# Kernel tuning notes

Measured on AMD Instinct MI355X. Metric: run time of the kernel, lower is better.

## Reference

```python
import jax, jax.numpy as jnp
import numpy as np

N_NODES = 50000
N_EDGES = 800000
N_GRAPHS = 128
IN_CH = 16
IN_CTX = 16
H_G = 128
H_C = 128
H_F = 128


def _lin_init(key, fan_in, fan_out):
    k1, k2 = jax.random.split(key)
    s = 1.0 / np.sqrt(fan_in)
    W = jax.random.uniform(k1, (fan_in, fan_out), minval=-s, maxval=s, dtype=jnp.float32)
    b = jax.random.uniform(k2, (fan_out,), minval=-s, maxval=s, dtype=jnp.float32)
    return W, b


def setup_inputs() -> dict:
    key = jax.random.key(0)
    ks = jax.random.split(key, 16)
    inp = {}
    inp['x'] = jax.random.normal(ks[0], (N_NODES, IN_CH), dtype=jnp.float32)
    inp['x_context'] = jax.random.normal(ks[1], (N_GRAPHS, IN_CTX), dtype=jnp.float32)
    inp['edge_index'] = jax.random.randint(ks[2], (2, N_EDGES), 0, N_NODES, dtype=jnp.int64)
    inp['batch'] = jnp.sort(jax.random.randint(ks[3], (N_NODES,), 0, N_GRAPHS, dtype=jnp.int64))
    inp['edge_weight'] = jax.random.uniform(ks[4], (N_EDGES,), dtype=jnp.float32)
    # graph conv weights (GCNConv): layer0 [IN_CH,H_G], layers1-3 [H_G,H_G]
    dims = [(IN_CH, H_G), (H_G, H_G), (H_G, H_G), (H_G, H_G)]
    for i, (di, do) in enumerate(dims):
        W, b = _lin_init(ks[5 + i], di, do)
        inp[f'gW{i}'] = W
        inp[f'gb{i}'] = b
    # context FC: [IN_CTX,H_C], [H_C,H_C], [H_C,H_C]
    cdims = [(IN_CTX, H_C), (H_C, H_C), (H_C, H_C)]
    for i, (di, do) in enumerate(cdims):
        W, b = _lin_init(ks[9 + i], di, do)
        inp[f'cW{i}'] = W
        inp[f'cb{i}'] = b
    # fc stack: [H_G+H_C,H_F], [H_F,H_F], [H_F,H_F]
    fdims = [(H_G + H_C, H_F), (H_F, H_F), (H_F, H_F)]
    for i, (di, do) in enumerate(fdims):
        W, b = _lin_init(ks[12 + i], di, do)
        inp[f'fW{i}'] = W
        inp[f'fb{i}'] = b
    return inp


def _forward(x, x_context, edge_index, batch, edge_weight,
             gWs, gbs, cWs, cbs, fWs, fbs):
    n = x.shape[0]
    src, dst = edge_index[0], edge_index[1]
    loop = jnp.arange(n, dtype=edge_index.dtype)
    # GCN: add self-loops with weight 1, symmetric normalization
    src_f = jnp.concatenate([src, loop])
    dst_f = jnp.concatenate([dst, loop])
    ew_f = jnp.concatenate([edge_weight, jnp.ones((n,), dtype=edge_weight.dtype)])
    deg = jax.ops.segment_sum(ew_f, dst_f, num_segments=n)
    dinv = jnp.where(deg > 0, jax.lax.rsqrt(jnp.where(deg > 0, deg, 1.0)), 0.0)
    norm = dinv[src_f] * ew_f * dinv[dst_f]  # [E+N]

    h = x
    for W, b in zip(gWs, gbs):
        hw = h @ W                                   # [N, H_G]
        msg = norm[:, None] * hw[src_f]              # gather + scale
        h = jax.ops.segment_sum(msg, dst_f, num_segments=n) + b
        h = jax.nn.relu(h)

    # global mean pool over graphs
    s = jax.ops.segment_sum(h, batch, num_segments=N_GRAPHS)
    cnt = jax.ops.segment_sum(jnp.ones((n,), dtype=h.dtype), batch, num_segments=N_GRAPHS)
    g = s / jnp.maximum(cnt, 1.0)[:, None]           # [G, H_G]

    c = x_context
    for W, b in zip(cWs, cbs):
        c = jax.nn.relu(c @ W + b)

    z = jnp.concatenate([g, c], axis=-1)             # [G, H_G + H_C]
    for W, b in zip(fWs[:-1], fbs[:-1]):
        z = jax.nn.relu(z @ W + b)
    z = z @ fWs[-1] + fbs[-1]
    return z


def reference(x, x_context, edge_index, batch, edge_weight,
              gW0, gb0, gW1, gb1, gW2, gb2, gW3, gb3,
              cW0, cb0, cW1, cb1, cW2, cb2,
              fW0, fb0, fW1, fb1, fW2, fb2):
    return _forward(x, x_context, edge_index, batch, edge_weight,
                    [gW0, gW1, gW2, gW3], [gb0, gb1, gb2, gb3],
                    [cW0, cW1, cW2], [cb0, cb1, cb2],
                    [fW0, fW1, fW2], [fb0, fb1, fb2])
```

## Files before the change

### kernel.cpp

```cpp
#include <hip/hip_runtime.h>

typedef __attribute__((ext_vector_type(8))) short short8;
typedef __attribute__((ext_vector_type(4))) float f32x4;

#define IN_CH 16
#define CAP 64

__device__ inline unsigned int bf16_rne(float f) {
  unsigned int u = __float_as_uint(f);
  unsigned int r = u + 0x7fffu + ((u >> 16) & 1u);
  return r >> 16;
}
__device__ inline float bf16lo(unsigned int g) { return __uint_as_float(g << 16); }
__device__ inline float bf16hi(unsigned int g) { return __uint_as_float(g & 0xffff0000u); }
__device__ inline short8 as_short8(uint4 u) {
  union { uint4 u; short8 s; } cv; cv.u = u; return cv.s;
}

__global__ void zero_kernel(int* __restrict__ cnt, int n) {
  int i = blockIdx.x * blockDim.x + threadIdx.x;
  for (int j = i; j < n; j += gridDim.x * blockDim.x) cnt[j] = 0;
}

__global__ void build_kernel(const int* __restrict__ ei, const float* __restrict__ ew,
                             int* __restrict__ cnt, int2* __restrict__ bucket, int E) {
  int e = blockIdx.x * blockDim.x + threadIdx.x;
  if (e < E) {
    int dst = ei[E + e];
    int old = atomicAdd(&cnt[dst], 1);
    if (old < CAP) {
      int2 p;
      p.x = ei[e];
      p.y = __float_as_int(ew[e]);
      bucket[(size_t)dst * CAP + old] = p;
    }
  }
}

__global__ __launch_bounds__(256) void node_prep_kernel(
    const int* __restrict__ cnt, const int2* __restrict__ bucket,
    const float* __restrict__ x, float* __restrict__ dinv,
    float* __restrict__ xs, int n) {
  int lane = threadIdx.x & 15;
  int v = blockIdx.x * 16 + (threadIdx.x >> 4);
  if (v >= n) return;
  int c = min(cnt[v], CAP);
  float s = 0.f;
  for (int j = lane; j < c; j += 16)
    s += __int_as_float(bucket[(size_t)v * CAP + j].y);
#pragma unroll
  for (int off = 1; off < 16; off <<= 1) s += __shfl_xor(s, off);
  float dv = rsqrtf(1.0f + s);
  if (lane == 0) dinv[v] = dv;
  xs[(size_t)v * 16 + lane] = dv * x[(size_t)v * 16 + lane];
}

__global__ __launch_bounds__(256) void spmm16_kernel(
    const float4* __restrict__ xs4, const float* __restrict__ dinv,
    const int* __restrict__ cnt, const int2* __restrict__ bucket,
    float4* __restrict__ A0_4, int n) {
  const int l = threadIdx.x & 63;
  const int q = l >> 2;
  const int c4 = l & 3;
  const int v = (blockIdx.x << 2) + (threadIdx.x >> 6);
  if (v >= n) return;
  const size_t beg = (size_t)v * CAP;
  const int c = min(cnt[v], CAP);
  float4 s = make_float4(0.f, 0.f, 0.f, 0.f);
  for (int j = 0; j < c; j += 16) {
    int jj = j + q;
    bool ok = jj < c;
    int2 p = bucket[ok ? beg + jj : beg];
    float w = ok ? __int_as_float(p.y) : 0.f;
    float4 u = xs4[(size_t)p.x * 4 + c4];
    s.x += w * u.x; s.y += w * u.y; s.z += w * u.z; s.w += w * u.w;
  }
#pragma unroll
  for (int off = 4; off < 64; off <<= 1) {
    s.x += __shfl_xor(s.x, off);
    s.y += __shfl_xor(s.y, off);
    s.z += __shfl_xor(s.z, off);
    s.w += __shfl_xor(s.w, off);
  }
  float dv = dinv[v];
  float4 self = xs4[(size_t)v * 4 + c4];
  if (q == 0) {
    float4 o;
    o.x = dv * (s.x + self.x);
    o.y = dv * (s.y + self.y);
    o.z = dv * (s.z + self.z);
    o.w = dv * (s.w + self.w);
    A0_4[(size_t)v * 4 + c4] = o;
  }
}

__global__ __launch_bounds__(256) void spmm_bf16_kernel(
    const uint4* __restrict__ Hs4, const float* __restrict__ dinv,
    const int* __restrict__ cnt, const int2* __restrict__ bucket,
    uint4* __restrict__ Ab4, int n) {
  const int l = threadIdx.x & 63;
  const int q = l >> 4;
  const int c16 = l & 15;
  const int v = (blockIdx.x << 2) + (threadIdx.x >> 6);
  if (v >= n) return;
  const size_t beg = (size_t)v * CAP;
  const int c = min(cnt[v], CAP);
  float s[8] = {};
  for (int j = 0; j < c; j += 16) {
#pragma unroll
    for (int i = 0; i < 4; ++i) {
      int jj = j + i * 4 + q;
      bool ok = jj < c;
      int2 p = bucket[ok ? beg + jj : beg];
      float w = ok ? __int_as_float(p.y) : 0.f;
      uint4 u = Hs4[(size_t)p.x * 16 + c16];
      s[0] += w * bf16lo(u.x); s[1] += w * bf16hi(u.x);
      s[2] += w * bf16lo(u.y); s[3] += w * bf16hi(u.y);
      s[4] += w * bf16lo(u.z); s[5] += w * bf16hi(u.z);
      s[6] += w * bf16lo(u.w); s[7] += w * bf16hi(u.w);
    }
  }
#pragma unroll
  for (int j = 0; j < 8; ++j) {
    s[j] += __shfl_xor(s[j], 16);
    s[j] += __shfl_xor(s[j], 32);
  }
  float dv = dinv[v];
  uint4 self = Hs4[(size_t)v * 16 + c16];
  float r0 = dv * (s[0] + bf16lo(self.x));
  float r1 = dv * (s[1] + bf16hi(self.x));
  float r2 = dv * (s[2] + bf16lo(self.y));
  float r3 = dv * (s[3] + bf16hi(self.y));
  float r4 = dv * (s[4] + bf16lo(self.z));
  float r5 = dv * (s[5] + bf16hi(self.z));
  float r6 = dv * (s[6] + bf16lo(self.w));
  float r7 = dv * (s[7] + bf16hi(self.w));
  if (q == 0) {
    uint4 o;
    o.x = bf16_rne(r0) | (bf16_rne(r1) << 16);
    o.y = bf16_rne(r2) | (bf16_rne(r3) << 16);
    o.z = bf16_rne(r4) | (bf16_rne(r5) << 16);
    o.w = bf16_rne(r6) | (bf16_rne(r7) << 16);
    Ab4[(size_t)v * 16 + c16] = o;
  }
}

__global__ __launch_bounds__(256) void gemm16_kernel(
    const float* __restrict__ X, const float* __restrict__ W,
    const float* __restrict__ bias, const float* __restrict__ dinv,
    unsigned int* __restrict__ Hb, int n) {
  __shared__ float Ws[16][128];
  __shared__ float Xs[32][16];
  const int tid = threadIdx.x;
  const int row0 = blockIdx.x * 32;

  for (int i = tid * 4; i < 16 * 128; i += 1024)
    *(float4*)&Ws[0][i] = *(const float4*)&W[i];
  for (int i = tid * 4; i < 32 * 16; i += 1024) {
    int r = i / 16, k = i % 16;
    int rr = row0 + r;
    float4 v = make_float4(0.f, 0.f, 0.f, 0.f);
    if (rr < n) v = *(const float4*)&X[(size_t)rr * 16 + k];
    *(float4*)&Xs[r][k] = v;
  }
  __syncthreads();

  const int tc = (tid & 31) * 4;
  const int tr = (tid >> 5) * 4;
  float acc[4][4] = {};
  for (int k = 0; k < 16; k += 4) {
    float4 xv[4];
#pragma unroll
    for (int r = 0; r < 4; ++r) xv[r] = *(const float4*)&Xs[tr + r][k];
    float4 wv[4];
#pragma unroll
    for (int kk = 0; kk < 4; ++kk) wv[kk] = *(const float4*)&Ws[k + kk][tc];
#pragma unroll
    for (int r = 0; r < 4; ++r) {
      float xr[4] = {xv[r].x, xv[r].y, xv[r].z, xv[r].w};
#pragma unroll
      for (int kk = 0; kk < 4; ++kk) {
        acc[r][0] += xr[kk] * wv[kk].x;
        acc[r][1] += xr[kk] * wv[kk].y;
        acc[r][2] += xr[kk] * wv[kk].z;
        acc[r][3] += xr[kk] * wv[kk].w;
      }
    }
  }

  float4 bv = *(const float4*)&bias[tc];
#pragma unroll
  for (int r = 0; r < 4; ++r) {
    int rr = row0 + tr + r;
    if (rr < n) {
      float dv = dinv[rr];
      float o0 = dv * fmaxf(acc[r][0] + bv.x, 0.f);
      float o1 = dv * fmaxf(acc[r][1] + bv.y, 0.f);
      float o2 = dv * fmaxf(acc[r][2] + bv.z, 0.f);
      float o3 = dv * fmaxf(acc[r][3] + bv.w, 0.f);
      uint2 st;
      st.x = bf16_rne(o0) | (bf16_rne(o1) << 16);
      st.y = bf16_rne(o2) | (bf16_rne(o3) << 16);
      *(uint2*)&Hb[(size_t)rr * 64 + (tc >> 1)] = st;
    }
  }
}

__global__ void prep_wt3_kernel(const float* __restrict__ W1, const float* __restrict__ W2,
                                const float* __restrict__ W3, unsigned int* __restrict__ Wt) {
  int gid = blockIdx.x * 256 + threadIdx.x;
  if (gid >= 3 * 128 * 64) return;
  int layer = gid >> 13;
  int idx = gid & 8191;
  const float* W = (layer == 0) ? W1 : (layer == 1) ? W2 : W3;
  int c = idx >> 6, kp = idx & 63;
  float f0 = W[(2 * kp) * 128 + c];
  float f1 = W[(2 * kp + 1) * 128 + c];
  Wt[gid] = bf16_rne(f0) | (bf16_rne(f1) << 16);
}

__global__ __launch_bounds__(256) void gemm_mfma_kernel(
    const unsigned int* __restrict__ Ab, const unsigned int* __restrict__ Wtb,
    const float* __restrict__ bias, const float* __restrict__ dinv, int scale_out,
    unsigned short* __restrict__ Hh, int n) {
  __shared__ unsigned int Wlds[128 * 68];
  const int tid = threadIdx.x;
  for (int idx = tid; idx < 128 * 16; idx += 256) {
    int row = idx >> 4, slot = idx & 15;
    uint4 v = ((const uint4*)Wtb)[idx];
    *(uint4*)&Wlds[row * 68 + slot * 4] = v;
  }
  __syncthreads();

  const int lane = tid & 63, wid = tid >> 6;
  const int r0 = blockIdx.x * 128 + wid * 32;
  const int rowA = r0 + (lane & 15);
  const int kgrp = lane >> 4;
  const uint4* Abase = (const uint4*)Ab;

  f32x4 acc[2][8] = {};
#pragma unroll
  for (int kstep = 0; kstep < 4; ++kstep) {
    short8 a[2];
#pragma unroll
    for (int rb = 0; rb < 2; ++rb)
      a[rb] = as_short8(Abase[(size_t)(rowA + rb * 16) * 16 + kstep * 4 + kgrp]);
#pragma unroll
    for (int cb = 0; cb < 8; ++cb) {
      short8 b = as_short8(*(const uint4*)&Wlds[(cb * 16 + (lane & 15)) * 68 + (kstep * 4 + kgrp) * 4]);
      acc[0][cb] = __builtin_amdgcn_mfma_f32_16x16x32_bf16(a[0], b, acc[0][cb], 0, 0, 0);
      acc[1][cb] = __builtin_amdgcn_mfma_f32_16x16x32_bf16(a[1], b, acc[1][cb], 0, 0, 0);
    }
  }

  const int rbase = kgrp * 4;
  float dsc[2][4];
#pragma unroll
  for (int rb = 0; rb < 2; ++rb)
#pragma unroll
    for (int i = 0; i < 4; ++i) {
      int row = r0 + rb * 16 + rbase + i;
      dsc[rb][i] = (scale_out && row < n) ? dinv[row] : 1.0f;
    }

#pragma unroll
  for (int cb = 0; cb < 8; ++cb) {
    int col = cb * 16 + (lane & 15);
    float bv = bias[col];
#pragma unroll
    for (int rb = 0; rb < 2; ++rb) {
#pragma unroll
      for (int i = 0; i < 4; ++i) {
        int row = r0 + rb * 16 + rbase + i;
        if (row < n) {
          float o = dsc[rb][i] * fmaxf(acc[rb][cb][i] + bv, 0.f);
          Hh[(size_t)row * 128 + col] = (unsigned short)bf16_rne(o);
        }
      }
    }
  }
}

__global__ __launch_bounds__(256) void pool_part_kernel(
    const unsigned int* __restrict__ Hb, const int* __restrict__ batch,
    float* __restrict__ gpp, int G, int n) {
  int b = blockIdx.x;
  int g = b >> 2, chunk = b & 3;
  int lo = 0, hi = n;
  while (lo < hi) { int mid = (lo + hi) >> 1; if (batch[mid] < g) lo = mid + 1; else hi = mid; }
  int start = lo;
  lo = start; hi = n;
  while (lo < hi) { int mid = (lo + hi) >> 1; if (batch[mid] < g + 1) lo = mid + 1; else hi = mid; }
  int end = lo;

  int lane = threadIdx.x & 63, grp = threadIdx.x >> 6;
  float s0 = 0.f, s1 = 0.f;
  for (int v = start + chunk * 4 + grp; v < end; v += 16) {
    unsigned int u = Hb[((size_t)v << 6) + lane];
    s0 += bf16lo(u);
    s1 += bf16hi(u);
  }
  __shared__ float red[4][128];
  red[grp][2 * lane] = s0;
  red[grp][2 * lane + 1] = s1;
  __syncthreads();
  if (threadIdx.x < 128) {
    float t = red[0][threadIdx.x] + red[1][threadIdx.x] + red[2][threadIdx.x] + red[3][threadIdx.x];
    gpp[((size_t)chunk * G + g) * 128 + threadIdx.x] = t;
  }
}

__device__ inline void mlp_layer(const float* __restrict__ Wg, const float* __restrict__ bg,
                                 const float* in_lds, float* out_lds, float* Wl,
                                 float (*psum)[128], int K, int tid, int do_relu) {
  __syncthreads();
  for (int i = tid * 4; i < K * 128; i += 1024)
    *(float4*)&Wl[i] = *(const float4*)&Wg[i];
  __syncthreads();
  int h = tid >> 7, c = tid & 127;
  int k0 = h * (K >> 1), k1 = k0 + (K >> 1);
  float s = 0.f;
#pragma unroll 4
  for (int k = k0; k < k1; ++k) s += in_lds[k] * Wl[k * 128 + c];
  psum[h][c] = s;
  __syncthreads();
  if (tid < 128) {
    float r = psum[0][c] + psum[1][c] + bg[c];
    out_lds[c] = do_relu ? fmaxf(r, 0.f) : r;
  }
}

__global__ __launch_bounds__(256) void ctx_head_kernel(
    const float* __restrict__ gpp, const int* __restrict__ batch,
    const float* __restrict__ xc,
    const float* __restrict__ cW0, const float* __restrict__ cb0,
    const float* __restrict__ cW1, const float* __restrict__ cb1,
    const float* __restrict__ cW2, const float* __restrict__ cb2,
    const float* __restrict__ fW0, const float* __restrict__ fb0,
    const float* __restrict__ fW1, const float* __restrict__ fb1,
    const float* __restrict__ fW2, const float* __restrict__ fb2,
    float* __restrict__ out, int G, int n) {
  __shared__ float Wl[256 * 128];
  __shared__ float zz[256];
  __shared__ float tA[128];
  __shared__ float tB[128];
  __shared__ float psum[2][128];
  __shared__ float xin[16];

  int g = blockIdx.x;
  int tid = threadIdx.x;

  int lo = 0, hi = n;
  while (lo < hi) { int mid = (lo + hi) >> 1; if (batch[mid] < g) lo = mid + 1; else hi = mid; }
  int start = lo;
  lo = start; hi = n;
  while (lo < hi) { int mid = (lo + hi) >> 1; if (batch[mid] < g + 1) lo = mid + 1; else hi = mid; }
  int end = lo;
  float inv_cnt = 1.0f / fmaxf((float)(end - start), 1.0f);

  if (tid < 128) {
    float t = gpp[((size_t)0 * G + g) * 128 + tid] + gpp[((size_t)1 * G + g) * 128 + tid] +
              gpp[((size_t)2 * G + g) * 128 + tid] + gpp[((size_t)3 * G + g) * 128 + tid];
    zz[tid] = t * inv_cnt;
  }
  if (tid < 16) xin[tid] = xc[g * 16 + tid];

  mlp_layer(cW0, cb0, xin, tA, Wl, psum, 16, tid, 1);
  mlp_layer(cW1, cb1, tA, tB, Wl, psum, 128, tid, 1);
  mlp_layer(cW2, cb2, tB, zz + 128, Wl, psum, 128, tid, 1);
  mlp_layer(fW0, fb0, zz, tA, Wl, psum, 256, tid, 1);
  mlp_layer(fW1, fb1, tA, tB, Wl, psum, 128, tid, 1);
  __syncthreads();
  for (int i = tid * 4; i < 128 * 128; i += 1024)
    *(float4*)&Wl[i] = *(const float4*)&fW2[i];
  __syncthreads();
  {
    int h = tid >> 7, c = tid & 127;
    int k0 = h * 64, k1 = k0 + 64;
    float s = 0.f;
#pragma unroll 4
    for (int k = k0; k < k1; ++k) s += tB[k] * Wl[k * 128 + c];
    psum[h][c] = s;
  }
  __syncthreads();
  if (tid < 128) {
    out[g * 128 + tid] = psum[0][tid] + psum[1][tid] + fb2[tid];
  }
}

extern "C" void kernel_launch(void* const* d_in, const int* in_sizes, int n_in,
                              void* d_out, int out_size, void* d_ws, size_t ws_size,
                              hipStream_t stream) {
  const float* x     = (const float*)d_in[0];
  const float* xc    = (const float*)d_in[1];
  const int*   ei    = (const int*)d_in[2];
  const int*   batch = (const int*)d_in[3];
  const float* ew    = (const float*)d_in[4];
  const float* gW[4] = {(const float*)d_in[5], (const float*)d_in[7], (const float*)d_in[9],  (const float*)d_in[11]};
  const float* gb[4] = {(const float*)d_in[6], (const float*)d_in[8], (const float*)d_in[10], (const float*)d_in[12]};
  const float* cW0 = (const float*)d_in[13]; const float* cb0 = (const float*)d_in[14];
  const float* cW1 = (const float*)d_in[15]; const float* cb1 = (const float*)d_in[16];
  const float* cW2 = (const float*)d_in[17]; const float* cb2 = (const float*)d_in[18];
  const float* fW0 = (const float*)d_in[19]; const float* fb0 = (const float*)d_in[20];
  const float* fW1 = (const float*)d_in[21]; const float* fb1 = (const float*)d_in[22];
  const float* fW2 = (const float*)d_in[23]; const float* fb2 = (const float*)d_in[24];
  float* out = (float*)d_out;

  const int N = in_sizes[3];
  const int E = in_sizes[4];
  const int G = in_sizes[1] / IN_CH;
  const int Np = (N + 127) & ~127;

  char* p = (char*)d_ws;
  auto alloc = [&](size_t bytes) { char* r = p; p += (bytes + 255) & ~(size_t)255; return r; };
  int*   cnt    = (int*)  alloc((size_t)N * 4);
  int2*  bucket = (int2*) alloc((size_t)N * CAP * 8);
  float* dinv   = (float*)alloc((size_t)N * 4);
  float* xs     = (float*)alloc((size_t)N * 16 * 4);
  float* A0     = (float*)alloc((size_t)N * 16 * 4);
  unsigned int* Ab = (unsigned int*)alloc((size_t)Np * 64 * 4);
  unsigned int* Hb = (unsigned int*)alloc((size_t)Np * 64 * 4);
  unsigned int* Wt = (unsigned int*)alloc((size_t)3 * 128 * 64 * 4);
  float* gpp = (float*)alloc((size_t)4 * G * 128 * 4);

  int nbE = (E + 255) / 256;

  zero_kernel<<<128, 256, 0, stream>>>(cnt, N);
  build_kernel<<<nbE, 256, 0, stream>>>(ei, ew, cnt, bucket, E);
  node_prep_kernel<<<(N + 15) / 16, 256, 0, stream>>>(cnt, bucket, x, dinv, xs, N);

  prep_wt3_kernel<<<96, 256, 0, stream>>>(gW[1], gW[2], gW[3], Wt);

  spmm16_kernel<<<(N + 3) / 4, 256, 0, stream>>>((const float4*)xs, dinv, cnt, bucket,
                                                 (float4*)A0, N);
  gemm16_kernel<<<(N + 31) / 32, 256, 0, stream>>>(A0, gW[0], gb[0], dinv, Hb, N);

  for (int l = 0; l < 3; ++l) {
    spmm_bf16_kernel<<<(N + 3) / 4, 256, 0, stream>>>((const uint4*)Hb, dinv, cnt, bucket,
                                                      (uint4*)Ab, N);
    gemm_mfma_kernel<<<Np / 128, 256, 0, stream>>>(Ab, Wt + (size_t)l * 8192, gb[l + 1], dinv,
                                                   (l < 2) ? 1 : 0, (unsigned short*)Hb, N);
  }

  pool_part_kernel<<<4 * G, 256, 0, stream>>>(Hb, batch, gpp, G, N);
  ctx_head_kernel<<<G, 256, 0, stream>>>(gpp, batch, xc, cW0, cb0, cW1, cb1, cW2, cb2,
                                         fW0, fb0, fW1, fb1, fW2, fb2, out, G, N);
}
```

Baseline: 302.7 us.

## Batch eight graphs per block in MLP head to reuse staged weights

Replaces the per-graph context/FC head kernel with one where each block handles eight graphs. Each weight tile is staged to LDS once and applied to all eight rows, with K processed in 128-row chunks so the LDS buffer shrinks to 64KB. This cuts redundant global weight loads and launches only 16 blocks instead of 128, trading parallelism for reuse. It relies on G being divisible by 8.

Measured after the change: 316.8 us. +4.7%, slower.

```diff
diff --git a/kernel.cpp b/kernel.cpp
--- a/kernel.cpp
+++ b/kernel.cpp
@@ -310,27 +310,51 @@
   }
 }
 
-__device__ inline void mlp_layer(const float* __restrict__ Wg, const float* __restrict__ bg,
-                                 const float* in_lds, float* out_lds, float* Wl,
-                                 float (*psum)[128], int K, int tid, int do_relu) {
-  __syncthreads();
-  for (int i = tid * 4; i < K * 128; i += 1024)
-    *(float4*)&Wl[i] = *(const float4*)&Wg[i];
-  __syncthreads();
-  int h = tid >> 7, c = tid & 127;
-  int k0 = h * (K >> 1), k1 = k0 + (K >> 1);
-  float s = 0.f;
-#pragma unroll 4
-  for (int k = k0; k < k1; ++k) s += in_lds[k] * Wl[k * 128 + c];
-  psum[h][c] = s;
-  __syncthreads();
-  if (tid < 128) {
-    float r = psum[0][c] + psum[1][c] + bg[c];
-    out_lds[c] = do_relu ? fmaxf(r, 0.f) : r;
-  }
-}
-
-__global__ __launch_bounds__(256) void ctx_head_kernel(
+__device__ inline void layer8(const float* __restrict__ Wg, const float* __restrict__ bg,
+                              const float* __restrict__ in, int instride,
+                              float* __restrict__ outp, int outstride,
+                              float* __restrict__ Wl, int K, int tid, int relu_,
+                              float* __restrict__ gout) {
+  int c = tid & 127, gh = tid >> 7;
+  float s0 = 0.f, s1 = 0.f, s2 = 0.f, s3 = 0.f;
+  for (int k0 = 0; k0 < K; k0 += 128) {
+    int KC = (K - k0 < 128) ? (K - k0) : 128;
+    __syncthreads();
+    for (int i = tid * 4; i < KC * 128; i += 1024)
+      *(float4*)&Wl[i] = *(const float4*)&Wg[(size_t)k0 * 128 + i];
+    __syncthreads();
+    const float* in0 = in + (gh * 4 + 0) * instride + k0;
+    const float* in1 = in + (gh * 4 + 1) * instride + k0;
+    const float* in2 = in + (gh * 4 + 2) * instride + k0;
+    const float* in3 = in + (gh * 4 + 3) * instride + k0;
+    for (int k = 0; k < KC; ++k) {
+      float w = Wl[k * 128 + c];
+      s0 += in0[k] * w;
+      s1 += in1[k] * w;
+      s2 += in2[k] * w;
+      s3 += in3[k] * w;
+    }
+  }
+  float b = bg[c];
+  s0 += b; s1 += b; s2 += b; s3 += b;
+  if (relu_) {
+    s0 = fmaxf(s0, 0.f); s1 = fmaxf(s1, 0.f);
+    s2 = fmaxf(s2, 0.f); s3 = fmaxf(s3, 0.f);
+  }
+  if (gout) {
+    gout[(gh * 4 + 0) * 128 + c] = s0;
+    gout[(gh * 4 + 1) * 128 + c] = s1;
+    gout[(gh * 4 + 2) * 128 + c] = s2;
+    gout[(gh * 4 + 3) * 128 + c] = s3;
+  } else {
+    outp[(gh * 4 + 0) * outstride + c] = s0;
+    outp[(gh * 4 + 1) * outstride + c] = s1;
+    outp[(gh * 4 + 2) * outstride + c] = s2;
+    outp[(gh * 4 + 3) * outstride + c] = s3;
+  }
+}
+
+__global__ __launch_bounds__(256) void tail_kernel(
     const float* __restrict__ gpp, const int* __restrict__ batch,
     const float* __restrict__ xc,
     const float* __restrict__ cW0, const float* __restrict__ cb0,
@@ -340,52 +364,48 @@
     const float* __restrict__ fW1, const float* __restrict__ fb1,
     const float* __restrict__ fW2, const float* __restrict__ fb2,
     float* __restrict__ out, int G, int n) {
-  __shared__ float Wl[256 * 128];
-  __shared__ float zz[256];
-  __shared__ float tA[128];
-  __shared__ float tB[128];
-  __shared__ float psum[2][128];
-  __shared__ float xin[16];
-
-  int g = blockIdx.x;
-  int tid = threadIdx.x;
-
-  int lo = 0, hi = n;
-  while (lo < hi) { int mid = (lo + hi) >> 1; if (batch[mid] < g) lo = mid + 1; else hi = mid; }
-  int start = lo;
-  lo = start; hi = n;
-  while (lo < hi) { int mid = (lo + hi) >> 1; if (batch[mid] < g + 1) lo = mid + 1; else hi = mid; }
-  int end = lo;
-  float inv_cnt = 1.0f / fmaxf((float)(end - start), 1.0f);
-
-  if (tid < 128) {
-    float t = gpp[((size_t)0 * G + g) * 128 + tid] + gpp[((size_t)1 * G + g) * 128 + tid] +
-              gpp[((size_t)2 * G + g) * 128 + tid] + gpp[((size_t)3 * G + g) * 128 + tid];
-    zz[tid] = t * inv_cnt;
-  }
-  if (tid < 16) xin[tid] = xc[g * 16 + tid];
-
-  mlp_layer(cW0, cb0, xin, tA, Wl, psum, 16, tid, 1);
-  mlp_layer(cW1, cb1, tA, tB, Wl, psum, 128, tid, 1);
-  mlp_layer(cW2, cb2, tB, zz + 128, Wl, psum, 128, tid, 1);
-  mlp_layer(fW0, fb0, zz, tA, Wl, psum, 256, tid, 1);
-  mlp_layer(fW1, fb1, tA, tB, Wl, psum, 128, tid, 1);
+  __shared__ float Wl[128 * 128];
+  __shared__ float z[8][256];
+  __shared__ float tA[8][128];
+  __shared__ float tB[8][128];
+  __shared__ float xin[8][16];
+  __shared__ float invc[8];
+
+  const int tid = threadIdx.x;
+  const int g0 = blockIdx.x * 8;
+
+  for (int i = tid; i < 8 * 128; i += 256) {
+    int gl = i >> 7, c = i & 127;
+    int g = g0 + gl;
+    float t = gpp[((size_t)0 * G + g) * 128 + c] + gpp[((size_t)1 * G + g) * 128 + c] +
+              gpp[((size_t)2 * G + g) * 128 + c] + gpp[((size_t)3 * G + g) * 128 + c];
+    z[gl][c] = t;
+  }
+  if (tid < 8) {
+    int g = g0 + tid;
+    int lo = 0, hi = n;
+    while (lo < hi) { int m = (lo + hi) >> 1; if (batch[m] < g) lo = m + 1; else hi = m; }
+    int st = lo;
+    lo = st; hi = n;
+    while (lo < hi) { int m = (lo + hi) >> 1; if (batch[m] < g + 1) lo = m + 1; else hi = m; }
+    invc[tid] = 1.0f / fmaxf((float)(lo - st), 1.0f);
+  }
+  for (int i = tid; i < 8 * 16; i += 256) {
+    int gl = i >> 4, c = i & 15;
+    xin[gl][c] = xc[(g0 + gl) * 16 + c];
+  }
   __syncthreads();
-  for (int i = tid * 4; i < 128 * 128; i += 1024)
-    *(float4*)&Wl[i] = *(const float4*)&fW2[i];
-  __syncthreads();
-  {
-    int h = tid >> 7, c = tid & 127;
-    int k0 = h * 64, k1 = k0 + 64;
-    float s = 0.f;
-#pragma unroll 4
-    for (int k = k0; k < k1; ++k) s += tB[k] * Wl[k * 128 + c];
-    psum[h][c] = s;
-  }
-  __syncthreads();
-  if (tid < 128) {
-    out[g * 128 + tid] = psum[0][tid] + psum[1][tid] + fb2[tid];
-  }
+  for (int i = tid; i < 8 * 128; i += 256) {
+    int gl = i >> 7, c = i & 127;
+    z[gl][c] *= invc[gl];
+  }
+
+  layer8(cW0, cb0, &xin[0][0], 16, &tA[0][0], 128, Wl, 16, tid, 1, nullptr);
+  layer8(cW1, cb1, &tA[0][0], 128, &tB[0][0], 128, Wl, 128, tid, 1, nullptr);
+  layer8(cW2, cb2, &tB[0][0], 128, &z[0][128], 256, Wl, 128, tid, 1, nullptr);
+  layer8(fW0, fb0, &z[0][0], 256, &tA[0][0], 128, Wl, 256, tid, 1, nullptr);
+  layer8(fW1, fb1, &tA[0][0], 128, &tB[0][0], 128, Wl, 128, tid, 1, nullptr);
+  layer8(fW2, fb2, &tB[0][0], 128, nullptr, 0, Wl, 128, tid, 0, out + (size_t)g0 * 128);
 }
 
 extern "C" void kernel_launch(void* const* d_in, const int* in_sizes, int n_in,
@@ -443,6 +463,6 @@
   }
 
   pool_part_kernel<<<4 * G, 256, 0, stream>>>(Hb, batch, gpp, G, N);
-  ctx_head_kernel<<<G, 256, 0, stream>>>(gpp, batch, xc, cW0, cb0, cW1, cb1, cW2, cb2,
+  tail_kernel<<<G / 8, 256, 0, stream>>>(gpp, batch, xc, cW0, cb0, cW1, cb1, cW2, cb2,
                                          fW0, fb0, fW1, fb1, fW2, fb2, out, G, N);
 }
```

## Transpose head MLP weights once and read them directly from global memory

Applied to the files above, without the earlier changes.

Adds a prep kernel that transposes all six context/FC weight matrices into a column-major buffer. The per-graph head kernel then reads weights straight from global memory with float4 dot products instead of staging each layer's full weight matrix into 128KB of LDS. It also overlaps the batch binary search with the gpp and x_context loads. This removes the LDS copy and its extra barriers and raises occupancy, at the cost of one more launch and relying on L2 to serve the weights shared by the 128 blocks.

After: 285.5 us. 1.06x faster.

```diff
diff --git a/kernel.cpp b/kernel.cpp
--- a/kernel.cpp
+++ b/kernel.cpp
@@ -219,6 +219,29 @@
   Wt[gid] = bf16_rne(f0) | (bf16_rne(f1) << 16);
 }
 
+#define TOFF1 2048
+#define TOFF2 (TOFF1 + 16384)
+#define TOFF3 (TOFF2 + 16384)
+#define TOFF4 (TOFF3 + 32768)
+#define TOFF5 (TOFF4 + 16384)
+#define TTOTAL (TOFF5 + 16384)
+__global__ void prep_tail_kernel(
+    const float* __restrict__ cW0, const float* __restrict__ cW1, const float* __restrict__ cW2,
+    const float* __restrict__ fW0, const float* __restrict__ fW1, const float* __restrict__ fW2,
+    float* __restrict__ WT) {
+  int gid = blockIdx.x * 256 + threadIdx.x;
+  if (gid >= TTOTAL) return;
+  const float* W; int lgK, idx;
+  if (gid < TOFF1)      { W = cW0; lgK = 4; idx = gid; }
+  else if (gid < TOFF2) { W = cW1; lgK = 7; idx = gid - TOFF1; }
+  else if (gid < TOFF3) { W = cW2; lgK = 7; idx = gid - TOFF2; }
+  else if (gid < TOFF4) { W = fW0; lgK = 8; idx = gid - TOFF3; }
+  else if (gid < TOFF5) { W = fW1; lgK = 7; idx = gid - TOFF4; }
+  else                  { W = fW2; lgK = 7; idx = gid - TOFF5; }
+  int c = idx >> lgK, k = idx & ((1 << lgK) - 1);
+  WT[gid] = W[k * 128 + c];
+}
+
 __global__ __launch_bounds__(256) void gemm_mfma_kernel(
     const unsigned int* __restrict__ Ab, const unsigned int* __restrict__ Wtb,
     const float* __restrict__ bias, const float* __restrict__ dinv, int scale_out,
@@ -310,82 +333,71 @@
   }
 }
 
-__device__ inline void mlp_layer(const float* __restrict__ Wg, const float* __restrict__ bg,
-                                 const float* in_lds, float* out_lds, float* Wl,
-                                 float (*psum)[128], int K, int tid, int do_relu) {
-  __syncthreads();
-  for (int i = tid * 4; i < K * 128; i += 1024)
-    *(float4*)&Wl[i] = *(const float4*)&Wg[i];
-  __syncthreads();
-  int h = tid >> 7, c = tid & 127;
-  int k0 = h * (K >> 1), k1 = k0 + (K >> 1);
-  float s = 0.f;
-#pragma unroll 4
-  for (int k = k0; k < k1; ++k) s += in_lds[k] * Wl[k * 128 + c];
-  psum[h][c] = s;
+__device__ inline void tlayer(const float* __restrict__ WTl, const float* __restrict__ bg,
+                              const float* in_lds, float* out_lds,
+                              float (*psum)[128], int K, int tid, int relu_,
+                              float* __restrict__ gout) {
+  const int c = tid & 127, kh = tid >> 7;
+  const int kcnt = K >> 1;
+  const float4* w4 = (const float4*)(WTl + (size_t)c * K + kh * kcnt);
+  const float4* i4 = (const float4*)(in_lds + kh * kcnt);
+  const int n4 = kcnt >> 2;
+  __syncthreads();
+  float acc = 0.f;
+#pragma unroll 8
+  for (int t = 0; t < n4; ++t) {
+    float4 wv = w4[t];
+    float4 iv = i4[t];
+    acc += iv.x * wv.x + iv.y * wv.y + iv.z * wv.z + iv.w * wv.w;
+  }
+  psum[kh][c] = acc;
   __syncthreads();
   if (tid < 128) {
     float r = psum[0][c] + psum[1][c] + bg[c];
-    out_lds[c] = do_relu ? fmaxf(r, 0.f) : r;
-  }
-}
-
-__global__ __launch_bounds__(256) void ctx_head_kernel(
+    if (relu_) r = fmaxf(r, 0.f);
+    if (gout) gout[c] = r; else out_lds[c] = r;
+  }
+}
+
+__global__ __launch_bounds__(256) void tail2_kernel(
     const float* __restrict__ gpp, const int* __restrict__ batch,
-    const float* __restrict__ xc,
-    const float* __restrict__ cW0, const float* __restrict__ cb0,
-    const float* __restrict__ cW1, const float* __restrict__ cb1,
-    const float* __restrict__ cW2, const float* __restrict__ cb2,
-    const float* __restrict__ fW0, const float* __restrict__ fb0,
-    const float* __restrict__ fW1, const float* __restrict__ fb1,
-    const float* __restrict__ fW2, const float* __restrict__ fb2,
+    const float* __restrict__ xc, const float* __restrict__ WT,
+    const float* __restrict__ cb0, const float* __restrict__ cb1, const float* __restrict__ cb2,
+    const float* __restrict__ fb0, const float* __restrict__ fb1, const float* __restrict__ fb2,
     float* __restrict__ out, int G, int n) {
-  __shared__ float Wl[256 * 128];
-  __shared__ float zz[256];
+  __shared__ float z[256];
   __shared__ float tA[128];
   __shared__ float tB[128];
+  __shared__ float xin[16];
   __shared__ float psum[2][128];
-  __shared__ float xin[16];
-
-  int g = blockIdx.x;
-  int tid = threadIdx.x;
-
-  int lo = 0, hi = n;
-  while (lo < hi) { int mid = (lo + hi) >> 1; if (batch[mid] < g) lo = mid + 1; else hi = mid; }
-  int start = lo;
-  lo = start; hi = n;
-  while (lo < hi) { int mid = (lo + hi) >> 1; if (batch[mid] < g + 1) lo = mid + 1; else hi = mid; }
-  int end = lo;
-  float inv_cnt = 1.0f / fmaxf((float)(end - start), 1.0f);
+  __shared__ float invc_sh;
+
+  const int g = blockIdx.x;
+  const int tid = threadIdx.x;
 
   if (tid < 128) {
     float t = gpp[((size_t)0 * G + g) * 128 + tid] + gpp[((size_t)1 * G + g) * 128 + tid] +
               gpp[((size_t)2 * G + g) * 128 + tid] + gpp[((size_t)3 * G + g) * 128 + tid];
-    zz[tid] = t * inv_cnt;
-  }
-  if (tid < 16) xin[tid] = xc[g * 16 + tid];
-
-  mlp_layer(cW0, cb0, xin, tA, Wl, psum, 16, tid, 1);
-  mlp_layer(cW1, cb1, tA, tB, Wl, psum, 128, tid, 1);
-  mlp_layer(cW2, cb2, tB, zz + 128, Wl, psum, 128, tid, 1);
-  mlp_layer(fW0, fb0, zz, tA, Wl, psum, 256, tid, 1);
-  mlp_layer(fW1, fb1, tA, tB, Wl, psum, 128, tid, 1);
-  __syncthreads();
-  for (int i = tid * 4; i < 128 * 128; i += 1024)
-    *(float4*)&Wl[i] = *(const float4*)&fW2[i];
-  __syncthreads();
-  {
-    int h = tid >> 7, c = tid & 127;
-    int k0 = h * 64, k1 = k0 + 64;
-    float s = 0.f;
-#pragma unroll 4
-    for (int k = k0; k < k1; ++k) s += tB[k] * Wl[k * 128 + c];
-    psum[h][c] = s;
-  }
-  __syncthreads();
-  if (tid < 128) {
-    out[g * 128 + tid] = psum[0][tid] + psum[1][tid] + fb2[tid];
-  }
+    z[tid] = t;
+  } else if (tid < 144) {
+    xin[tid - 128] = xc[g * 16 + (tid - 128)];
+  } else if (tid == 144) {
+    int lo = 0, hi = n;
+    while (lo < hi) { int m = (lo + hi) >> 1; if (batch[m] < g) lo = m + 1; else hi = m; }
+    int st = lo;
+    lo = st; hi = n;
+    while (lo < hi) { int m = (lo + hi) >> 1; if (batch[m] < g + 1) lo = m + 1; else hi = m; }
+    invc_sh = 1.0f / fmaxf((float)(lo - st), 1.0f);
+  }
+  __syncthreads();
+  if (tid < 128) z[tid] *= invc_sh;
+
+  tlayer(WT,          cb0, xin, tA,      psum, 16,  tid, 1, nullptr);
+  tlayer(WT + TOFF1,  cb1, tA,  tB,      psum, 128, tid, 1, nullptr);
+  tlayer(WT + TOFF2,  cb2, tB,  z + 128, psum, 128, tid, 1, nullptr);
+  tlayer(WT + TOFF3,  fb0, z,   tA,      psum, 256, tid, 1, nullptr);
+  tlayer(WT + TOFF4,  fb1, tA,  tB,      psum, 128, tid, 1, nullptr);
+  tlayer(WT + TOFF5,  fb2, tB,  nullptr, psum, 128, tid, 0, out + (size_t)g * 128);
 }
 
 extern "C" void kernel_launch(void* const* d_in, const int* in_sizes, int n_in,
@@ -421,6 +433,7 @@
   unsigned int* Ab = (unsigned int*)alloc((size_t)Np * 64 * 4);
   unsigned int* Hb = (unsigned int*)alloc((size_t)Np * 64 * 4);
   unsigned int* Wt = (unsigned int*)alloc((size_t)3 * 128 * 64 * 4);
+  float* WT  = (float*)alloc((size_t)TTOTAL * 4);
   float* gpp = (float*)alloc((size_t)4 * G * 128 * 4);
 
   int nbE = (E + 255) / 256;
@@ -430,6 +443,7 @@
   node_prep_kernel<<<(N + 15) / 16, 256, 0, stream>>>(cnt, bucket, x, dinv, xs, N);
 
   prep_wt3_kernel<<<96, 256, 0, stream>>>(gW[1], gW[2], gW[3], Wt);
+  prep_tail_kernel<<<(TTOTAL + 255) / 256, 256, 0, stream>>>(cW0, cW1, cW2, fW0, fW1, fW2, WT);
 
   spmm16_kernel<<<(N + 3) / 4, 256, 0, stream>>>((const float4*)xs, dinv, cnt, bucket,
                                                  (float4*)A0, N);
@@ -443,6 +457,6 @@
   }
 
   pool_part_kernel<<<4 * G, 256, 0, stream>>>(Hb, batch, gpp, G, N);
-  ctx_head_kernel<<<G, 256, 0, stream>>>(gpp, batch, xc, cW0, cb0, cW1, cb1, cW2, cb2,
-                                         fW0, fb0, fW1, fb1, fW2, fb2, out, G, N);
-}
+  tail2_kernel<<<G, 256, 0, stream>>>(gpp, batch, xc, WT, cb0, cb1, cb2,
+                                      fb0, fb1, fb2, out, G, N);
+}
```
